# Optimization experiments

Measured on AMD Instinct MI355X. Metric: run time of the kernel, lower is better.

Reference implementation:

```python
import jax, jax.numpy as jnp
import numpy as np

N_NODES = 50000
N_EDGES = 800000
N_GRAPHS = 32
D = 300
NUM_CLASSES = 40


def setup_inputs() -> dict:
    key = jax.random.key(0)
    ks = jax.random.split(key, 32)

    def w(k, shape):
        fan_in = shape[-2]
        return (jax.random.normal(k, shape, jnp.float32) / np.sqrt(fan_in)).astype(jnp.float32)

    inp = {
        'x': jax.random.normal(ks[0], (N_NODES, 3), jnp.float32),
        'edge_index': jax.random.randint(ks[1], (2, N_EDGES), 0, N_NODES, jnp.int32),
        'batch': jnp.sort(jax.random.randint(ks[2], (N_NODES,), 0, N_GRAPHS, jnp.int32)),
        # project MLP [3, 64, 128, 300]
        'pW1': w(ks[3], (3, 64)),   'pb1': jnp.zeros((64,), jnp.float32),
        'pW2': w(ks[4], (64, 128)), 'pb2': jnp.zeros((128,), jnp.float32),
        'pW3': w(ks[5], (128, D)),  'pb3': jnp.zeros((D,), jnp.float32),
        # 3 PointGNNConv layers, params stacked on leading axis
        'hW': w(ks[6], (3, D, 3)),      'hb': jnp.zeros((3, 3), jnp.float32),
        'fW': w(ks[7], (3, D + 3, D)),  'fb': jnp.zeros((3, D), jnp.float32),
        'gW': w(ks[8], (3, D, D)),      'gb': jnp.zeros((3, D), jnp.float32),
        # 3 post-conv linear layers [300, 300]
        'lW': w(ks[9], (3, D, D)),      'lb': jnp.zeros((3, D), jnp.float32),
        # decision head
        'dW': w(ks[10], (D, NUM_CLASSES)), 'db': jnp.zeros((NUM_CLASSES,), jnp.float32),
    }
    return inp


def reference(x, edge_index, batch, pW1, pb1, pW2, pb2, pW3, pb3,
              hW, hb, fW, fb, gW, gb, lW, lb, dW, db):
    pos = x  # [N, 3] raw point coordinates
    src, dst = edge_index[0], edge_index[1]  # j -> i (source_to_target)

    # embed MLP (eval mode: dropout/batchnorm are identity)
    h = jax.nn.relu(x @ pW1 + pb1)
    h = jax.nn.relu(h @ pW2 + pb2)
    h = h @ pW3 + pb3  # [N, 300]

    for i in range(3):
        # PointGNNConv: delta = mlp_h(x_i); e = mlp_f([pos_j - pos_i + delta_i, x_j]); max-aggr; mlp_g + residual
        delta = h @ hW[i] + hb[i]                     # [N, 3]
        rel = pos[src] - pos[dst] + delta[dst]        # [E, 3]
        e = jnp.concatenate([rel, h[src]], axis=1) @ fW[i] + fb[i]  # [E, 300]
        agg = jax.ops.segment_max(e, dst, num_segments=N_NODES)    # [N, 300]
        agg = jnp.where(jnp.isfinite(agg), agg, 0.0)  # zero-degree nodes -> 0
        h = agg @ gW[i] + gb[i] + h                   # residual
        h = jax.nn.relu(h)
        h = h @ lW[i] + lb[i]                         # lin_i

    # global mean pool over graphs
    sums = jax.ops.segment_sum(h, batch, num_segments=N_GRAPHS)           # [G, 300]
    cnt = jax.ops.segment_sum(jnp.ones((h.shape[0],), h.dtype), batch, num_segments=N_GRAPHS)
    mean = sums / jnp.maximum(cnt, 1.0)[:, None]

    logits = mean @ dW + db  # [G, 40]
    return jax.nn.log_softmax(logits, axis=1)
```

## Files before the change

### kernel.cpp

```cpp
#include <hip/hip_runtime.h>
#include <hip/hip_bf16.h>

#define DD 300
#define DP 320

typedef unsigned short ushort_t;
typedef __attribute__((ext_vector_type(8))) short short8;
typedef __attribute__((ext_vector_type(4))) float f32x4;

__device__ __forceinline__ float b2f(ushort_t u) {
    unsigned x = ((unsigned)u) << 16;
    return __uint_as_float(x);
}
__device__ __forceinline__ ushort_t f2b(float f) {
    unsigned u = __float_as_uint(f);
    unsigned r = (u + 0x7FFFu + ((u >> 16) & 1u)) >> 16;
    return (ushort_t)r;
}

__device__ __forceinline__ void gload16(const void* g, void* l) {
    __builtin_amdgcn_global_load_lds((const __attribute__((address_space(1))) void*)g,
                                     (__attribute__((address_space(3))) void*)l, 16, 0, 0);
}

template<int BNT, int BIAS, int RELU, int RESID, int RANK3>
__launch_bounds__(512)
__global__ void gemm_mfma(const ushort_t* __restrict__ A, int strideA, int M, int K,
                          const ushort_t* __restrict__ Bt,
                          const float* __restrict__ bias,
                          const ushort_t* __restrict__ resid,
                          const float* __restrict__ X3,
                          const float* __restrict__ W3,
                          int NCOL,
                          ushort_t* __restrict__ C, int strideC)
{
    constexpr int BM = 128, BK = 64, BN = 32 * BNT;
    constexpr int CA = BM * BK * 2 / 1024;
    constexpr int CB = BN * BK * 2 / 1024;
    constexpr int WCOLS = 16 * BNT;
    __shared__ ushort_t As[2][BM * BK];
    __shared__ ushort_t Bs[2][BN * BK];

    int bx = blockIdx.x, by = blockIdx.y;
    if (gridDim.x == 2 && (gridDim.y & 7) == 0) {
        int flat = bx + (by << 1);
        int xcd = flat & 7;
        int slot = flat >> 3;
        int rpx = gridDim.y >> 3;
        by = xcd * rpx + (slot >> 1);
        bx = slot & 1;
    }

    const int tid = threadIdx.x;
    const int lane = tid & 63, wid = tid >> 6;
    const int rowTile = by * BM;
    const int colTile = bx * BN;
    const int wm = wid >> 1, wn = wid & 1;

    const int lrow = lane >> 3;
    const int l8b = (lane & 7) * 16;

    f32x4 acc[2][BNT];
    #pragma unroll
    for (int f = 0; f < 2; ++f)
        #pragma unroll
        for (int q = 0; q < BNT; ++q) {
            f32x4 z = {0.f, 0.f, 0.f, 0.f};
            acc[f][q] = z;
        }

    auto stage = [&](int buf, int k0) {
        for (int c = wid; c < CA; c += 8) {
            int row = c * 8 + lrow;
            int colb = l8b ^ ((row & 7) << 4);
            int gr = rowTile + row; if (gr > M - 1) gr = M - 1;
            gload16(A + (size_t)gr * strideA + k0 + (colb >> 1), &As[buf][c * 512]);
        }
        for (int c = wid; c < CB; c += 8) {
            int row = c * 8 + lrow;
            int colb = l8b ^ ((row & 7) << 4);
            gload16(Bt + (size_t)(colTile + row) * K + k0 + (colb >> 1), &Bs[buf][c * 512]);
        }
    };

    auto compute = [&](int buf) {
        #pragma unroll
        for (int ks = 0; ks < 2; ++ks) {
            const int kidx = ks * 32 + (lane >> 4) * 8;
            short8 af[2], bf[BNT];
            #pragma unroll
            for (int f = 0; f < 2; ++f) {
                int row = wm * 32 + f * 16 + (lane & 15);
                int phys = (row * 128 + kidx * 2) ^ ((row & 7) << 4);
                af[f] = *(const short8*)((const char*)&As[buf][0] + phys);
            }
            #pragma unroll
            for (int q = 0; q < BNT; ++q) {
                int row = wn * WCOLS + q * 16 + (lane & 15);
                int phys = (row * 128 + kidx * 2) ^ ((row & 7) << 4);
                bf[q] = *(const short8*)((const char*)&Bs[buf][0] + phys);
            }
            #pragma unroll
            for (int f = 0; f < 2; ++f)
                #pragma unroll
                for (int q = 0; q < BNT; ++q)
                    acc[f][q] = __builtin_amdgcn_mfma_f32_16x16x32_bf16(af[f], bf[q], acc[f][q], 0, 0, 0);
        }
    };

    const int NT = K / BK;
    stage(0, 0);
    asm volatile("s_waitcnt vmcnt(0)" ::: "memory");
    __builtin_amdgcn_s_barrier();

    int cur = 0;
    for (int t = 0; t < NT - 1; ++t) {
        stage(cur ^ 1, (t + 1) * BK);
        compute(cur);
        asm volatile("s_waitcnt vmcnt(0)" ::: "memory");
        __builtin_amdgcn_s_barrier();
        cur ^= 1;
    }
    compute(cur);

    ushort_t* eb = &Bs[cur ^ 1][0] + wid * 16 * WCOLS;
    #pragma unroll
    for (int f = 0; f < 2; ++f) {
        #pragma unroll
        for (int q = 0; q < BNT; ++q) {
            #pragma unroll
            for (int r = 0; r < 4; ++r) {
                int rl = (lane >> 4) * 4 + r;
                int row = rowTile + wm * 32 + f * 16 + rl;
                int rr = row < M ? row : M - 1;
                int col = colTile + wn * WCOLS + q * 16 + (lane & 15);
                float v = acc[f][q][r];
                if (BIAS) v += bias[col];
                if (RANK3) {
                    if (col < NCOL) {
                        v += X3[rr * 3 + 0] * W3[col]
                           + X3[rr * 3 + 1] * W3[NCOL + col]
                           + X3[rr * 3 + 2] * W3[2 * NCOL + col];
                    }
                }
                if (RESID) v += b2f(resid[(size_t)rr * strideC + col]);
                if (RELU) v = fmaxf(v, 0.f);
                eb[rl * WCOLS + q * 16 + (lane & 15)] = f2b(v);
            }
        }
        for (int ch = lane; ch < 32 * BNT; ch += 64) {
            int rl = ch / (2 * BNT);
            int cc = ch - rl * (2 * BNT);
            int row = rowTile + wm * 32 + f * 16 + rl;
            if (row < M) {
                short8 vv = *(const short8*)(eb + rl * WCOLS + cc * 8);
                *(short8*)(C + (size_t)row * strideC + colTile + wn * WCOLS + cc * 8) = vv;
            }
        }
    }
}

__global__ void prep(const float* __restrict__ pW2, const float* __restrict__ pW3,
                     const float* __restrict__ pb3,
                     const float* __restrict__ hW, const float* __restrict__ hb,
                     const float* __restrict__ fW,
                     const float* __restrict__ gW, const float* __restrict__ gb,
                     const float* __restrict__ lW, const float* __restrict__ lb,
                     ushort_t* __restrict__ WU, ushort_t* __restrict__ WG,
                     ushort_t* __restrict__ WL, ushort_t* __restrict__ W2,
                     ushort_t* __restrict__ W3e,
                     float* __restrict__ bU, float* __restrict__ bG,
                     float* __restrict__ bL, float* __restrict__ b3)
{
    const int SZ = DP * DP;
    int idx = blockIdx.x * 256 + threadIdx.x;
    if (idx < 3 * SZ) {
        int i = idx / SZ, r = idx - i * SZ;
        int n = r / DP, k = r - n * DP;
        float v = 0.f;
        if (k < DD) {
            if (n < DD) v = fW[i * 90900 + (3 + k) * DD + n];
            else if (n < DD + 3) v = hW[i * 900 + k * 3 + (n - DD)];
        }
        WU[idx] = f2b(v);
        return;
    }
    idx -= 3 * SZ;
    if (idx < 3 * SZ) {
        int i = idx / SZ, r = idx - i * SZ;
        int n = r / DP, k = r - n * DP;
        float v = (n < DD && k < DD) ? gW[i * 90000 + k * DD + n] : 0.f;
        WG[idx] = f2b(v);
        return;
    }
    idx -= 3 * SZ;
    if (idx < 3 * SZ) {
        int i = idx / SZ, r = idx - i * SZ;
        int n = r / DP, k = r - n * DP;
        float v = (n < DD && k < DD) ? lW[i * 90000 + k * DD + n] : 0.f;
        WL[idx] = f2b(v);
        return;
    }
    idx -= 3 * SZ;
    if (idx < 128 * 64) {
        int n = idx >> 6, k = idx & 63;
        W2[idx] = f2b(pW2[k * 128 + n]);
        return;
    }
    idx -= 128 * 64;
    if (idx < DP * 128) {
        int n = idx >> 7, k = idx & 127;
        W3e[idx] = f2b((n < DD) ? pW3[k * DD + n] : 0.f);
        return;
    }
    idx -= DP * 128;
    if (idx < 3 * DP) {
        int i = idx / DP, n = idx - i * DP;
        bU[idx] = (n >= DD && n < DD + 3) ? hb[i * 3 + (n - DD)] : 0.f;
        return;
    }
    idx -= 3 * DP;
    if (idx < 3 * DP) {
        int i = idx / DP, n = idx - i * DP;
        bG[idx] = (n < DD) ? gb[i * DD + n] : 0.f;
        return;
    }
    idx -= 3 * DP;
    if (idx < 3 * DP) {
        int i = idx / DP, n = idx - i * DP;
        bL[idx] = (n < DD) ? lb[i * DD + n] : 0.f;
        return;
    }
    idx -= 3 * DP;
    if (idx < DP) {
        b3[idx] = (idx < DD) ? pb3[idx] : 0.f;
        return;
    }
}

__global__ void embed1(const float* __restrict__ x, const float* __restrict__ W,
                       const float* __restrict__ b, ushort_t* __restrict__ h1, int M)
{
    int idx = blockIdx.x * 256 + threadIdx.x;
    if (idx >= M * 64) return;
    int n = idx >> 6, c = idx & 63;
    const float* xr = x + n * 3;
    float v = xr[0] * W[c] + xr[1] * W[64 + c] + xr[2] * W[128 + c] + b[c];
    h1[idx] = f2b(fmaxf(v, 0.f));
}

__global__ void hist_kernel(const int* __restrict__ dst, int* __restrict__ cnt, int E)
{
    int e = blockIdx.x * 256 + threadIdx.x;
    if (e < E) atomicAdd(&cnt[dst[e]], 1);
}
__global__ void scan1(const int* __restrict__ cnt, int* __restrict__ bsum, int N)
{
    __shared__ int s[256];
    int t = threadIdx.x;
    int i = blockIdx.x * 256 + t;
    s[t] = (i < N) ? cnt[i] : 0;
    __syncthreads();
    for (int o = 128; o > 0; o >>= 1) { if (t < o) s[t] += s[t + o]; __syncthreads(); }
    if (t == 0) bsum[blockIdx.x] = s[0];
}
__global__ void scan2(int* __restrict__ bsum, int nb)
{
    __shared__ int s[256];
    int t = threadIdx.x;
    int v = (t < nb) ? bsum[t] : 0;
    s[t] = v; __syncthreads();
    for (int o = 1; o < 256; o <<= 1) {
        int x = (t >= o) ? s[t - o] : 0;
        __syncthreads();
        s[t] += x;
        __syncthreads();
    }
    if (t < nb) bsum[t] = s[t] - v;
}
__global__ void scan3(const int* __restrict__ cnt, const int* __restrict__ bsumx,
                      int* __restrict__ off, int* __restrict__ cursor, int N)
{
    __shared__ int s[256];
    int t = threadIdx.x;
    int i = blockIdx.x * 256 + t;
    int v = (i < N) ? cnt[i] : 0;
    s[t] = v; __syncthreads();
    for (int o = 1; o < 256; o <<= 1) {
        int x = (t >= o) ? s[t - o] : 0;
        __syncthreads();
        s[t] += x;
        __syncthreads();
    }
    int excl = s[t] - v + bsumx[blockIdx.x];
    if (i <= N) {
        off[i] = excl;
        if (i < N) cursor[i] = excl;
    }
}
__global__ void scatter_kernel(const int* __restrict__ src, const int* __restrict__ dst,
                               int* __restrict__ cursor, int* __restrict__ csr, int E)
{
    int e = blockIdx.x * 256 + threadIdx.x;
    if (e < E) {
        int p = atomicAdd(&cursor[dst[e]], 1);
        csr[p] = src[e];
    }
}

__global__ void segmax(const ushort_t* __restrict__ u, const int* __restrict__ off,
                       const int* __restrict__ csr,
                       const float* __restrict__ x, const float* __restrict__ fWp,
                       const float* __restrict__ fb, ushort_t* __restrict__ agg, int Nn)
{
    int n = blockIdx.x * 4 + (threadIdx.x >> 6);
    int lane = threadIdx.x & 63;
    if (n >= Nn) return;
    const int e0 = off[n], e1 = off[n + 1];

    const ushort_t* un = u + (size_t)n * DP;
    float d0 = b2f(un[300]) - x[n * 3 + 0];
    float d1 = b2f(un[301]) - x[n * 3 + 1];
    float d2 = b2f(un[302]) - x[n * 3 + 2];

    float m[5];
    #pragma unroll
    for (int j = 0; j < 5; ++j) m[j] = -INFINITY;

    int e = e0;
    for (; e + 7 < e1; e += 8) {
        int s[8];
        #pragma unroll
        for (int q = 0; q < 8; ++q) s[q] = csr[e + q];
        #pragma unroll
        for (int q = 0; q < 8; ++q) {
            const ushort_t* r = u + (size_t)s[q] * DP + lane;
            #pragma unroll
            for (int j = 0; j < 5; ++j) m[j] = fmaxf(m[j], b2f(r[64 * j]));
        }
    }
    for (; e + 3 < e1; e += 4) {
        int s[4];
        #pragma unroll
        for (int q = 0; q < 4; ++q) s[q] = csr[e + q];
        #pragma unroll
        for (int q = 0; q < 4; ++q) {
            const ushort_t* r = u + (size_t)s[q] * DP + lane;
            #pragma unroll
            for (int j = 0; j < 5; ++j) m[j] = fmaxf(m[j], b2f(r[64 * j]));
        }
    }
    for (; e < e1; ++e) {
        const ushort_t* r = u + (size_t)csr[e] * DP + lane;
        #pragma unroll
        for (int j = 0; j < 5; ++j) m[j] = fmaxf(m[j], b2f(r[64 * j]));
    }

    #pragma unroll
    for (int j = 0; j < 5; ++j) {
        int col = lane + 64 * j;
        float o = 0.f;
        if (e1 > e0 && col < DD)
            o = m[j] + fb[col] + d0 * fWp[col] + d1 * fWp[DD + col] + d2 * fWp[2 * DD + col];
        agg[(size_t)n * DP + col] = f2b(o);
    }
}

__global__ void pool_kernel(const ushort_t* __restrict__ h, const int* __restrict__ batch,
                            float* __restrict__ sums, float* __restrict__ cnts,
                            int Nn, int npb)
{
    int c = threadIdx.x;
    int n0 = blockIdx.x * npb;
    int n1 = min(n0 + npb, Nn);
    if (n0 >= n1) return;
    if (c < DD) {
        float run = 0.f;
        int g = batch[n0];
        for (int n = n0; n < n1; ++n) {
            int gn = batch[n];
            if (gn != g) { atomicAdd(&sums[g * DD + c], run); run = 0.f; g = gn; }
            run += b2f(h[(size_t)n * DP + c]);
        }
        atomicAdd(&sums[g * DD + c], run);
    } else if (c == DD) {
        float run = 0.f;
        int g = batch[n0];
        for (int n = n0; n < n1; ++n) {
            int gn = batch[n];
            if (gn != g) { atomicAdd(&cnts[g], run); run = 0.f; g = gn; }
            run += 1.f;
        }
        atomicAdd(&cnts[g], run);
    }
}

__global__ void head_kernel(const float* __restrict__ sums, const float* __restrict__ cnts,
                            const float* __restrict__ dW, const float* __restrict__ db,
                            float* __restrict__ out)
{
    __shared__ float mean[32][DD];
    __shared__ float logits[32][40];
    int tid = threadIdx.x;
    for (int i = tid; i < 32 * DD; i += 256) {
        int g = i / DD;
        mean[g][i - g * DD] = sums[i] / fmaxf(cnts[g], 1.f);
    }
    __syncthreads();
    for (int o = tid; o < 32 * 40; o += 256) {
        int g = o / 40, cls = o - g * 40;
        float acc = db[cls];
        for (int k = 0; k < DD; ++k) acc += mean[g][k] * dW[k * 40 + cls];
        logits[g][cls] = acc;
    }
    __syncthreads();
    if (tid < 32) {
        float mx = -INFINITY;
        #pragma unroll
        for (int j = 0; j < 40; ++j) mx = fmaxf(mx, logits[tid][j]);
        float se = 0.f;
        for (int j = 0; j < 40; ++j) se += expf(logits[tid][j] - mx);
        float lse = mx + logf(se);
        for (int j = 0; j < 40; ++j) out[tid * 40 + j] = logits[tid][j] - lse;
    }
}

extern "C" void kernel_launch(void* const* d_in, const int* in_sizes, int n_in,
                              void* d_out, int out_size, void* d_ws, size_t ws_size,
                              hipStream_t stream)
{
    const float* x     = (const float*)d_in[0];
    const int*   ei    = (const int*)d_in[1];
    const int*   batch = (const int*)d_in[2];
    const float* pW1   = (const float*)d_in[3];
    const float* pb1   = (const float*)d_in[4];
    const float* pW2   = (const float*)d_in[5];
    const float* pb2   = (const float*)d_in[6];
    const float* pW3   = (const float*)d_in[7];
    const float* pb3   = (const float*)d_in[8];
    const float* hW    = (const float*)d_in[9];
    const float* hb    = (const float*)d_in[10];
    const float* fW    = (const float*)d_in[11];
    const float* fb    = (const float*)d_in[12];
    const float* gW    = (const float*)d_in[13];
    const float* gb    = (const float*)d_in[14];
    const float* lW    = (const float*)d_in[15];
    const float* lb    = (const float*)d_in[16];
    const float* dW    = (const float*)d_in[17];
    const float* db    = (const float*)d_in[18];

    const int N = in_sizes[0] / 3;
    const int E = in_sizes[1] / 2;
    const int G = 32;
    const int SZ = DP * DP;
    (void)ws_size; (void)n_in; (void)out_size;

    char* wsb = (char*)d_ws;
    size_t offb = 0;
    auto alloc = [&](size_t bytes) {
        void* p = wsb + offb;
        offb += (bytes + 255) & ~(size_t)255;
        return p;
    };
    ushort_t* h    = (ushort_t*)alloc((size_t)N * DP * 2);
    ushort_t* u    = (ushort_t*)alloc((size_t)N * DP * 2);
    ushort_t* agg  = (ushort_t*)alloc((size_t)N * DP * 2);
    ushort_t* h1   = (ushort_t*)alloc((size_t)N * 64 * 2);
    ushort_t* h2   = (ushort_t*)alloc((size_t)N * 128 * 2);
    ushort_t* WU   = (ushort_t*)alloc((size_t)3 * SZ * 2);
    ushort_t* WG   = (ushort_t*)alloc((size_t)3 * SZ * 2);
    ushort_t* WL   = (ushort_t*)alloc((size_t)3 * SZ * 2);
    ushort_t* W2   = (ushort_t*)alloc((size_t)128 * 64 * 2);
    ushort_t* W3e  = (ushort_t*)alloc((size_t)DP * 128 * 2);
    float*    bU   = (float*)alloc((size_t)3 * DP * 4);
    float*    bG   = (float*)alloc((size_t)3 * DP * 4);
    float*    bL   = (float*)alloc((size_t)3 * DP * 4);
    float*    b3   = (float*)alloc((size_t)DP * 4);
    int*      cnt    = (int*)alloc((size_t)(N + 1) * 4);
    int*      offp   = (int*)alloc((size_t)(N + 1) * 4);
    int*      cursor = (int*)alloc((size_t)N * 4);
    int*      bsum   = (int*)alloc((size_t)256 * 4);
    int*      csr    = (int*)alloc((size_t)E * 4);
    float*    sums   = (float*)alloc((size_t)(G * DD + G) * 4);
    float*    cnts   = sums + G * DD;

    const int* srcp = ei;
    const int* dstp = ei + E;
    const int nb = (N + 255) / 256;
    const dim3 blk(256);
    const int rowBlocks = (N + 127) / 128;
    const int rowBlocksPad = ((rowBlocks + 7) / 8) * 8;

    const int prepTotal = 3 * SZ * 3 + 128 * 64 + DP * 128 + 3 * DP * 3 + DP;
    prep<<<dim3((prepTotal + 255) / 256), blk, 0, stream>>>(
        pW2, pW3, pb3, hW, hb, fW, gW, gb, lW, lb,
        WU, WG, WL, W2, W3e, bU, bG, bL, b3);

    hipMemsetAsync(cnt, 0, (size_t)(N + 1) * 4, stream);
    hist_kernel<<<dim3((E + 255) / 256), blk, 0, stream>>>(dstp, cnt, E);
    scan1<<<dim3(nb), blk, 0, stream>>>(cnt, bsum, N);
    scan2<<<dim3(1), blk, 0, stream>>>(bsum, nb);
    scan3<<<dim3(nb), blk, 0, stream>>>(cnt, bsum, offp, cursor, N);
    scatter_kernel<<<dim3((E + 255) / 256), blk, 0, stream>>>(srcp, dstp, cursor, csr, E);

    embed1<<<dim3((N * 64 + 255) / 256), blk, 0, stream>>>(x, pW1, pb1, h1, N);
    gemm_mfma<4, 1, 1, 0, 0><<<dim3(1, rowBlocks), dim3(512), 0, stream>>>(
        h1, 64, N, 64, W2, pb2, nullptr, nullptr, nullptr, 128, h2, 128);
    gemm_mfma<5, 1, 0, 0, 0><<<dim3(2, rowBlocksPad), dim3(512), 0, stream>>>(
        h2, 128, N, 128, W3e, b3, nullptr, nullptr, nullptr, DD, h, DP);

    for (int i = 0; i < 3; ++i) {
        const float* fWi = fW + (size_t)i * 90900;
        const float* fbi = fb + (size_t)i * DD;

        gemm_mfma<5, 1, 0, 0, 1><<<dim3(2, rowBlocksPad), dim3(512), 0, stream>>>(
            h, DP, N, DP, WU + (size_t)i * SZ, bU + (size_t)i * DP,
            nullptr, x, fWi, DD, u, DP);

        segmax<<<dim3((N + 3) / 4), blk, 0, stream>>>(u, offp, csr, x, fWi, fbi, agg, N);

        gemm_mfma<5, 1, 1, 1, 0><<<dim3(2, rowBlocksPad), dim3(512), 0, stream>>>(
            agg, DP, N, DP, WG + (size_t)i * SZ, bG + (size_t)i * DP,
            h, nullptr, nullptr, DD, u, DP);

        gemm_mfma<5, 1, 0, 0, 0><<<dim3(2, rowBlocksPad), dim3(512), 0, stream>>>(
            u, DP, N, DP, WL + (size_t)i * SZ, bL + (size_t)i * DP,
            nullptr, nullptr, nullptr, DD, h, DP);
    }

    hipMemsetAsync(sums, 0, (size_t)(G * DD + G) * 4, stream);
    pool_kernel<<<dim3((N + 127) / 128), dim3(320), 0, stream>>>(h, batch, sums, cnts, N, 128);
    head_kernel<<<dim3(1), dim3(256), 0, stream>>>(sums, cnts, dW, db, (float*)d_out);
}
```

Baseline: 667.7 us.

## Fuse per-layer g, lin, and next-layer u GEMMs into one kernel

Adds a layer_fused kernel that keeps a 64-row tile in shared memory and chains three GEMMs: the g-MLP with residual and ReLU, the post-conv linear, and the next layer's u projection with its position term. This removes the global round-trips of intermediate activations and two launches per layer. In exchange the weight tiles are re-staged per 64-row block with synchronous waits and no double buffering, and the shared footprint is large. hin and hout alias the same buffer, which stays safe only because each block reads its residual rows before writing them.

```diff
diff --git a/kernel.cpp b/kernel.cpp
--- a/kernel.cpp
+++ b/kernel.cpp
@@ -157,6 +157,188 @@
                 *(short8*)(C + (size_t)row * strideC + colTile + wn * WCOLS + cc * 8) = vv;
             }
         }
+    }
+}
+
+template<int HASC>
+__launch_bounds__(512, 4)
+__global__ void layer_fused(const ushort_t* __restrict__ agg,
+                            const ushort_t* __restrict__ hin,
+                            const ushort_t* __restrict__ WG, const float* __restrict__ bG,
+                            const ushort_t* __restrict__ WL, const float* __restrict__ bL,
+                            const ushort_t* __restrict__ WU, const float* __restrict__ bU,
+                            const float* __restrict__ x, const float* __restrict__ fWn,
+                            ushort_t* __restrict__ hout, ushort_t* __restrict__ uout,
+                            int M)
+{
+    constexpr int BM = 64, BK = 32;
+    __shared__ ushort_t T[BM * DP];
+    __shared__ ushort_t Bst[DP * BK];
+    __shared__ ushort_t Ast[BM * BK];
+
+    const int tid = threadIdx.x;
+    const int lane = tid & 63, wid = tid >> 6;
+    const int rowTile = blockIdx.x * BM;
+    const int wm = wid >> 2, wn = wid & 3;
+
+    f32x4 acc[2][5];
+    auto zacc = [&]() {
+        #pragma unroll
+        for (int f = 0; f < 2; ++f)
+            #pragma unroll
+            for (int q = 0; q < 5; ++q) {
+                f32x4 z = {0.f, 0.f, 0.f, 0.f};
+                acc[f][q] = z;
+            }
+    };
+
+    auto stageB32 = [&](const ushort_t* W, int k0) {
+        for (int c = wid; c < 20; c += 8) {
+            int row = c * 16 + (lane >> 2);
+            int cole = (((lane & 3) ^ (row & 3)) << 3);
+            gload16(W + (size_t)row * DP + k0 + cole, Bst + c * 512);
+        }
+    };
+    auto stageA32 = [&](int k0) {
+        for (int c = wid; c < 4; c += 8) {
+            int row = c * 16 + (lane >> 2);
+            int cole = (((lane & 3) ^ (row & 3)) << 3);
+            int gr = rowTile + row; if (gr > M - 1) gr = M - 1;
+            gload16(agg + (size_t)gr * DP + k0 + cole, Ast + c * 512);
+        }
+    };
+
+    auto stepAB = [&]() {
+        const int ks = lane >> 4;
+        short8 af[2], bf[5];
+        #pragma unroll
+        for (int f = 0; f < 2; ++f) {
+            int row = wm * 32 + f * 16 + (lane & 15);
+            af[f] = *(const short8*)((const char*)Ast + row * 64 + ((ks ^ (row & 3)) << 4));
+        }
+        #pragma unroll
+        for (int q = 0; q < 5; ++q) {
+            int row = wn * 80 + q * 16 + (lane & 15);
+            bf[q] = *(const short8*)((const char*)Bst + row * 64 + ((ks ^ (row & 3)) << 4));
+        }
+        #pragma unroll
+        for (int f = 0; f < 2; ++f)
+            #pragma unroll
+            for (int q = 0; q < 5; ++q)
+                acc[f][q] = __builtin_amdgcn_mfma_f32_16x16x32_bf16(af[f], bf[q], acc[f][q], 0, 0, 0);
+    };
+
+    auto stepTB = [&](int k0) {
+        const int ksl = lane >> 4;
+        const int ksg = (k0 >> 3) + ksl;
+        short8 af[2], bf[5];
+        #pragma unroll
+        for (int f = 0; f < 2; ++f) {
+            int row = wm * 32 + f * 16 + (lane & 15);
+            af[f] = *(const short8*)((const char*)T + row * 640 + ((ksg ^ (row & 7)) << 4));
+        }
+        #pragma unroll
+        for (int q = 0; q < 5; ++q) {
+            int row = wn * 80 + q * 16 + (lane & 15);
+            bf[q] = *(const short8*)((const char*)Bst + row * 64 + ((ksl ^ (row & 3)) << 4));
+        }
+        #pragma unroll
+        for (int f = 0; f < 2; ++f)
+            #pragma unroll
+            for (int q = 0; q < 5; ++q)
+                acc[f][q] = __builtin_amdgcn_mfma_f32_16x16x32_bf16(af[f], bf[q], acc[f][q], 0, 0, 0);
+    };
+
+    auto twrite = [&](int row, int col, float v) {
+        *(ushort_t*)((char*)T + row * 640 + (((col >> 3) ^ (row & 7)) << 4) + ((col & 7) << 1)) = f2b(v);
+    };
+
+    auto copyOut = [&](ushort_t* out) {
+        for (int ch = tid; ch < BM * 40; ch += 512) {
+            int row = ch / 40, slot = ch - row * 40;
+            int grow = rowTile + row;
+            if (grow < M) {
+                short8 v = *(const short8*)((const char*)T + row * 640 + ((slot ^ (row & 7)) << 4));
+                *(short8*)(out + (size_t)grow * DP + slot * 8) = v;
+            }
+        }
+    };
+
+    zacc();
+    for (int t = 0; t < 10; ++t) {
+        if (t) __builtin_amdgcn_s_barrier();
+        stageA32(t * BK);
+        stageB32(WG, t * BK);
+        asm volatile("s_waitcnt vmcnt(0)" ::: "memory");
+        __builtin_amdgcn_s_barrier();
+        stepAB();
+    }
+    #pragma unroll
+    for (int f = 0; f < 2; ++f)
+        #pragma unroll
+        for (int q = 0; q < 5; ++q)
+            #pragma unroll
+            for (int r = 0; r < 4; ++r) {
+                int row = wm * 32 + f * 16 + (lane >> 4) * 4 + r;
+                int grow = rowTile + row;
+                int rr = grow < M ? grow : M - 1;
+                int col = wn * 80 + q * 16 + (lane & 15);
+                float v = acc[f][q][r] + bG[col] + b2f(hin[(size_t)rr * DP + col]);
+                twrite(row, col, fmaxf(v, 0.f));
+            }
+    __builtin_amdgcn_s_barrier();
+
+    zacc();
+    for (int t = 0; t < 10; ++t) {
+        if (t) __builtin_amdgcn_s_barrier();
+        stageB32(WL, t * BK);
+        asm volatile("s_waitcnt vmcnt(0)" ::: "memory");
+        __builtin_amdgcn_s_barrier();
+        stepTB(t * BK);
+    }
+    __builtin_amdgcn_s_barrier();
+    #pragma unroll
+    for (int f = 0; f < 2; ++f)
+        #pragma unroll
+        for (int q = 0; q < 5; ++q)
+            #pragma unroll
+            for (int r = 0; r < 4; ++r) {
+                int row = wm * 32 + f * 16 + (lane >> 4) * 4 + r;
+                int col = wn * 80 + q * 16 + (lane & 15);
+                twrite(row, col, acc[f][q][r] + bL[col]);
+            }
+    __builtin_amdgcn_s_barrier();
+    copyOut(hout);
+
+    if (HASC) {
+        zacc();
+        for (int t = 0; t < 10; ++t) {
+            if (t) __builtin_amdgcn_s_barrier();
+            stageB32(WU, t * BK);
+            asm volatile("s_waitcnt vmcnt(0)" ::: "memory");
+            __builtin_amdgcn_s_barrier();
+            stepTB(t * BK);
+        }
+        __builtin_amdgcn_s_barrier();
+        #pragma unroll
+        for (int f = 0; f < 2; ++f)
+            #pragma unroll
+            for (int q = 0; q < 5; ++q)
+                #pragma unroll
+                for (int r = 0; r < 4; ++r) {
+                    int row = wm * 32 + f * 16 + (lane >> 4) * 4 + r;
+                    int grow = rowTile + row;
+                    int rr = grow < M ? grow : M - 1;
+                    int col = wn * 80 + q * 16 + (lane & 15);
+                    float v = acc[f][q][r] + bU[col];
+                    if (col < DD)
+                        v += x[rr * 3 + 0] * fWn[col]
+                           + x[rr * 3 + 1] * fWn[DD + col]
+                           + x[rr * 3 + 2] * fWn[2 * DD + col];
+                    twrite(row, col, v);
+                }
+        __builtin_amdgcn_s_barrier();
+        copyOut(uout);
     }
 }
 
@@ -490,6 +672,7 @@
     const dim3 blk(256);
     const int rowBlocks = (N + 127) / 128;
     const int rowBlocksPad = ((rowBlocks + 7) / 8) * 8;
+    const int fuseBlocks = (N + 63) / 64;
 
     const int prepTotal = 3 * SZ * 3 + 128 * 64 + DP * 128 + 3 * DP * 3 + DP;
     prep<<<dim3((prepTotal + 255) / 256), blk, 0, stream>>>(
@@ -509,23 +692,31 @@
     gemm_mfma<5, 1, 0, 0, 0><<<dim3(2, rowBlocksPad), dim3(512), 0, stream>>>(
         h2, 128, N, 128, W3e, b3, nullptr, nullptr, nullptr, DD, h, DP);
 
+    gemm_mfma<5, 1, 0, 0, 1><<<dim3(2, rowBlocksPad), dim3(512), 0, stream>>>(
+        h, DP, N, DP, WU, bU, nullptr, x, fW, DD, u, DP);
+
     for (int i = 0; i < 3; ++i) {
         const float* fWi = fW + (size_t)i * 90900;
         const float* fbi = fb + (size_t)i * DD;
 
-        gemm_mfma<5, 1, 0, 0, 1><<<dim3(2, rowBlocksPad), dim3(512), 0, stream>>>(
-            h, DP, N, DP, WU + (size_t)i * SZ, bU + (size_t)i * DP,
-            nullptr, x, fWi, DD, u, DP);
-
         segmax<<<dim3((N + 3) / 4), blk, 0, stream>>>(u, offp, csr, x, fWi, fbi, agg, N);
 
-        gemm_mfma<5, 1, 1, 1, 0><<<dim3(2, rowBlocksPad), dim3(512), 0, stream>>>(
-            agg, DP, N, DP, WG + (size_t)i * SZ, bG + (size_t)i * DP,
-            h, nullptr, nullptr, DD, u, DP);
-
-        gemm_mfma<5, 1, 0, 0, 0><<<dim3(2, rowBlocksPad), dim3(512), 0, stream>>>(
-            u, DP, N, DP, WL + (size_t)i * SZ, bL + (size_t)i * DP,
-            nullptr, nullptr, nullptr, DD, h, DP);
+        if (i < 2) {
+            layer_fused<1><<<dim3(fuseBlocks), dim3(512), 0, stream>>>(
+                agg, h,
+                WG + (size_t)i * SZ, bG + (size_t)i * DP,
+                WL + (size_t)i * SZ, bL + (size_t)i * DP,
+                WU + (size_t)(i + 1) * SZ, bU + (size_t)(i + 1) * DP,
+                x, fW + (size_t)(i + 1) * 90900,
+                h, u, N);
+        } else {
+            layer_fused<0><<<dim3(fuseBlocks), dim3(512), 0, stream>>>(
+                agg, h,
+                WG + (size_t)i * SZ, bG + (size_t)i * DP,
+                WL + (size_t)i * SZ, bL + (size_t)i * DP,
+                nullptr, nullptr, nullptr, nullptr,
+                h, nullptr, N);
+        }
     }
 
     hipMemsetAsync(sums, 0, (size_t)(G * DD + G) * 4, stream);
```

Measured after the change: 783.4 us. 17.3% more time.
